# Kernel optimization log

Measured on AMD Instinct MI355X. Metric: run time of the kernel, lower is better.

The kernel has to match this reference:

```python
import jax, jax.numpy as jnp
import numpy as np

B, L, C, OUT = 8, 256, 512, 512


def setup_inputs() -> dict:
    key = jax.random.key(0)
    ks = jax.random.split(key, 8)
    xd = jax.random.normal(ks[0], (B, L, C), jnp.float32)
    xt = jax.random.normal(ks[1], (B, L, C), jnp.float32)
    # Linear weights stored (in, out): y = x @ W + b (equiv. to torch x @ W^T)
    Wc = jax.random.normal(ks[2], (C, C), jnp.float32) * 0.02
    bc = jnp.zeros((C,), jnp.float32)
    Wp = jax.random.normal(ks[3], (C, C), jnp.float32) * 0.02
    bp = jnp.zeros((C,), jnp.float32)
    Wf = jax.random.normal(ks[4], (C, OUT), jnp.float32) * 0.02
    bf = jnp.zeros((OUT,), jnp.float32)
    return {"xd": xd, "xt": xt, "Wc": Wc, "bc": bc, "Wp": Wp, "bp": bp, "Wf": Wf, "bf": bf}


def reference(xd, xt, Wc, bc, Wp, bp, Wf, bf):
    # projected features
    pt = jax.nn.relu(xt) @ Wp + bp              # (b, Lt, C)
    pc = jax.nn.relu(xd) @ Wc + bc              # (b, Ld, C)
    # sigmoid bilinear scores: (b, Lt, Ld) == (b, Ld, Lt) since Lt == Ld structurally
    scores = jax.nn.sigmoid(jnp.einsum('bic,bkc->bik', pt, pc))
    # normalize by total per-batch sum
    w = scores / jnp.sum(scores, axis=(1, 2), keepdims=True)
    # tanh of elementwise outer product, reduced with attention weights
    # cp[b,c] = sum_{i,j} tanh(xd[b,i,c] * xt[b,j,c]) * w[b,i,j]
    cp = jnp.einsum('bijc,bij->bc', jnp.tanh(xd[:, :, None, :] * xt[:, None, :, :]), w)
    return cp @ Wf + bf
```

## Files before the change

### kernel.cpp

```cpp
#include <hip/hip_runtime.h>
#include <math.h>

#define B_   8
#define L_   256
#define C_   512
#define OUT_ 512

typedef _Float16 half8 __attribute__((ext_vector_type(8)));
typedef _Float16 half4 __attribute__((ext_vector_type(4)));
typedef float    f32x4 __attribute__((ext_vector_type(4)));
typedef float    f32x2 __attribute__((ext_vector_type(2)));

__global__ __launch_bounds__(256)
void proj_mfma_kernel(const float* __restrict__ xt, const float* __restrict__ Wp,
                      const float* __restrict__ bp,
                      const float* __restrict__ xd, const float* __restrict__ Wc,
                      const float* __restrict__ bc,
                      _Float16* __restrict__ pt, _Float16* __restrict__ pc)
{
    const int which = blockIdx.z;
    const float* __restrict__ X    = which ? xd : xt;
    const float* __restrict__ W    = which ? Wc : Wp;
    const float* __restrict__ bias = which ? bc : bp;
    _Float16*    __restrict__ Y    = which ? pc : pt;

    __shared__ _Float16 Ah[2][64][40];
    __shared__ _Float16 Bh[2][64][40];
    __shared__ _Float16 Ot[64][72];

    const int tid = threadIdx.x;
    const int m0 = blockIdx.y << 6, n0 = blockIdx.x << 6;
    const int lane = tid & 63, wv = tid >> 6;
    const int l15 = lane & 15, quad = lane >> 4;

    const int srow = tid >> 2, sch = (tid & 3) << 3;
    const float* Ag = X + (size_t)(m0 + srow) * C_ + sch;
    const int nl = tid & 63, kseg = tid >> 6;
    const float* Bg = W + (size_t)(kseg << 3) * C_ + n0 + nl;

    float4 a0 = *(const float4*)(Ag);
    float4 a1 = *(const float4*)(Ag + 4);
    float wr[8];
    #pragma unroll
    for (int r = 0; r < 8; ++r) wr[r] = Bg[(size_t)r * C_];

    {
        half8 av;
        av[0] = (_Float16)fmaxf(a0.x, 0.f); av[1] = (_Float16)fmaxf(a0.y, 0.f);
        av[2] = (_Float16)fmaxf(a0.z, 0.f); av[3] = (_Float16)fmaxf(a0.w, 0.f);
        av[4] = (_Float16)fmaxf(a1.x, 0.f); av[5] = (_Float16)fmaxf(a1.y, 0.f);
        av[6] = (_Float16)fmaxf(a1.z, 0.f); av[7] = (_Float16)fmaxf(a1.w, 0.f);
        *(half8*)&Ah[0][srow][sch] = av;
        half8 bv;
        #pragma unroll
        for (int r = 0; r < 8; ++r) bv[r] = (_Float16)wr[r];
        *(half8*)&Bh[0][nl][kseg << 3] = bv;
    }

    f32x4 acc[4] = {};
    for (int ks = 0; ks < 16; ++ks) {
        const int cur = ks & 1;
        if (ks < 15) {
            Ag += 32;
            Bg += 32 * C_;
            a0 = *(const float4*)(Ag);
            a1 = *(const float4*)(Ag + 4);
            #pragma unroll
            for (int r = 0; r < 8; ++r) wr[r] = Bg[(size_t)r * C_];
        }
        __syncthreads();
        half8 af = *(const half8*)&Ah[cur][(wv << 4) + l15][quad << 3];
        #pragma unroll
        for (int nb = 0; nb < 4; ++nb) {
            half8 bf = *(const half8*)&Bh[cur][(nb << 4) + l15][quad << 3];
            acc[nb] = __builtin_amdgcn_mfma_f32_16x16x32_f16(af, bf, acc[nb], 0, 0, 0);
        }
        if (ks < 15) {
            half8 av;
            av[0] = (_Float16)fmaxf(a0.x, 0.f); av[1] = (_Float16)fmaxf(a0.y, 0.f);
            av[2] = (_Float16)fmaxf(a0.z, 0.f); av[3] = (_Float16)fmaxf(a0.w, 0.f);
            av[4] = (_Float16)fmaxf(a1.x, 0.f); av[5] = (_Float16)fmaxf(a1.y, 0.f);
            av[6] = (_Float16)fmaxf(a1.z, 0.f); av[7] = (_Float16)fmaxf(a1.w, 0.f);
            *(half8*)&Ah[cur ^ 1][srow][sch] = av;
            half8 bv;
            #pragma unroll
            for (int r = 0; r < 8; ++r) bv[r] = (_Float16)wr[r];
            *(half8*)&Bh[cur ^ 1][nl][kseg << 3] = bv;
        }
    }

    __syncthreads();
    #pragma unroll
    for (int nb = 0; nb < 4; ++nb) {
        const float bz = bias[n0 + (nb << 4) + l15];
        #pragma unroll
        for (int r = 0; r < 4; ++r)
            Ot[(wv << 4) + (quad << 2) + r][(nb << 4) + l15] = (_Float16)(acc[nb][r] + bz);
    }
    __syncthreads();
    const int erow = tid >> 3, ech = (tid & 7) << 3;
    #pragma unroll
    for (int h = 0; h < 64; h += 32)
        *(half8*)&Y[(size_t)(m0 + erow + h) * C_ + n0 + ech] = *(const half8*)&Ot[erow + h][ech];
}

__device__ __forceinline__ float sigmoid_fast(float z) {
    float e = __builtin_amdgcn_exp2f(-1.4426950408889634f * z);
    return __builtin_amdgcn_rcpf(e + 1.0f);
}

__global__ __launch_bounds__(512, 4)
void cp_scores_kernel(const _Float16* __restrict__ pt, const _Float16* __restrict__ pc,
                      const float* __restrict__ xd, const float* __restrict__ xt,
                      float* __restrict__ partials, float* __restrict__ sums_part)
{
    const int bx = blockIdx.x, by = blockIdx.y, b = blockIdx.z;
    const int i0 = bx << 5, j0 = by << 5;
    const int tid = threadIdx.x;
    const int lane = tid & 63, wv = tid >> 6;
    const int l15 = lane & 15, quad = lane >> 4;

    __shared__ _Float16 Ah[2][32][40];
    __shared__ _Float16 Bh[2][32][40];
    __shared__ float ws_[32][36];
    __shared__ float wred[4];

    const int sHalf = tid >> 8;
    const int srow  = (tid & 255) >> 3;
    const int sch   = (tid & 7) << 2;
    const _Float16* Sg = (sHalf ? pc + (size_t)(b * L_ + j0 + srow) * C_
                                : pt + (size_t)(b * L_ + i0 + srow) * C_) + sch;

    half4 v = *(const half4*)Sg;
    if (sHalf) *(half4*)&Bh[0][srow][sch] = v; else *(half4*)&Ah[0][srow][sch] = v;

    f32x4 acc = {};
    for (int ks = 0; ks < 16; ++ks) {
        const int cur = ks & 1;
        if (ks < 15) { Sg += 32; v = *(const half4*)Sg; }
        __syncthreads();
        if (wv < 4) {
            half8 af = *(const half8*)&Ah[cur][((wv >> 1) << 4) + l15][quad << 3];
            half8 bf = *(const half8*)&Bh[cur][((wv & 1) << 4) + l15][quad << 3];
            acc = __builtin_amdgcn_mfma_f32_16x16x32_f16(af, bf, acc, 0, 0, 0);
        }
        if (ks < 15) {
            if (sHalf) *(half4*)&Bh[cur ^ 1][srow][sch] = v;
            else       *(half4*)&Ah[cur ^ 1][srow][sch] = v;
        }
    }

    float lsum = 0.f;
    if (wv < 4) {
        const int n = ((wv & 1) << 4) + l15;
        const int m = ((wv >> 1) << 4) + (quad << 2);
        float4 sg;
        sg.x = sigmoid_fast(acc[0]);
        sg.y = sigmoid_fast(acc[1]);
        sg.z = sigmoid_fast(acc[2]);
        sg.w = sigmoid_fast(acc[3]);
        *(float4*)&ws_[n][m] = sg;
        lsum = (sg.x + sg.y) + (sg.z + sg.w);
    }
    #pragma unroll
    for (int off = 32; off; off >>= 1) lsum += __shfl_xor(lsum, off);
    if (wv < 4 && lane == 0) wred[wv] = lsum;
    __syncthreads();
    if (tid == 0)
        sums_part[(b << 6) | (bx << 3) | by] = (wred[0] + wred[1]) + (wred[2] + wred[3]);

    const int c = tid;
    const float* __restrict__ xdb = xd + (size_t)(b * L_ + i0) * C_ + c;
    const float* __restrict__ xtb = xt + (size_t)(b * L_ + j0) * C_ + c;
    f32x2 xds2[16];
    float xtv[32];
    #pragma unroll
    for (int i = 0; i < 16; ++i) {
        xds2[i].x = xdb[(size_t)(2 * i) * C_]     * 2.8853900817779268f;
        xds2[i].y = xdb[(size_t)(2 * i + 1) * C_] * 2.8853900817779268f;
    }
    #pragma unroll
    for (int j = 0; j < 32; ++j)
        xtv[j] = xtb[(size_t)j * C_];

    f32x2 acc01 = {0.f, 0.f}, acc23 = {0.f, 0.f};
    for (int jj = 0; jj < 32; ++jj) {
        const float xv = xtv[jj];
        #pragma unroll
        for (int i = 0; i < 32; i += 4) {
            const float4 w4 = *(const float4*)&ws_[jj][i];
            f32x2 x01 = xds2[i >> 1] * xv;
            f32x2 e01 = { __builtin_amdgcn_exp2f(x01.x), __builtin_amdgcn_exp2f(x01.y) };
            f32x2 q01 = e01 + 1.0f;
            float rp01 = __builtin_amdgcn_rcpf(q01.x * q01.y);
            f32x2 r01 = rp01 * __builtin_shufflevector(q01, q01, 1, 0);
            f32x2 w01 = { w4.x, w4.y };
            acc01 = w01 * r01 + acc01;
            f32x2 x23 = xds2[(i >> 1) + 1] * xv;
            f32x2 e23 = { __builtin_amdgcn_exp2f(x23.x), __builtin_amdgcn_exp2f(x23.y) };
            f32x2 q23 = e23 + 1.0f;
            float rp23 = __builtin_amdgcn_rcpf(q23.x * q23.y);
            f32x2 r23 = rp23 * __builtin_shufflevector(q23, q23, 1, 0);
            f32x2 w23 = { w4.z, w4.w };
            acc23 = w23 * r23 + acc23;
        }
    }
    const int p = (bx << 3) | by;
    partials[(size_t)((b << 6) | p) * C_ + c] =
        (acc01.x + acc01.y) + (acc23.x + acc23.y);
}

__global__ __launch_bounds__(512)
void finalize_kernel(const float* __restrict__ partials, const float* __restrict__ sums_part,
                     const float* __restrict__ Wf, const float* __restrict__ bfv,
                     float* __restrict__ out)
{
    const int b = blockIdx.y;
    const int t = threadIdx.x;
    __shared__ float cp[C_];
    __shared__ float red[512];
    __shared__ float sumsh;

    red[t] = (t < 64) ? sums_part[(b << 6) | t] : 0.f;

    float s = 0.f;
    #pragma unroll
    for (int p = 0; p < 64; ++p)
        s += partials[(size_t)((b << 6) | p) * C_ + t];

    __syncthreads();
    for (int st = 256; st > 0; st >>= 1) {
        if (t < st) red[t] += red[t + st];
        __syncthreads();
    }
    if (t == 0) sumsh = red[0];
    __syncthreads();

    cp[t] = 1.0f - 2.0f * s / sumsh;
    __syncthreads();

    const int o  = ((int)blockIdx.x << 6) | (t & 63);
    const int c0 = (t >> 6) << 6;
    float acc = 0.f;
    #pragma unroll 8
    for (int i = 0; i < 64; ++i) {
        const int cc = c0 + i;
        acc = fmaf(cp[cc], Wf[(size_t)cc * OUT_ + o], acc);
    }
    red[t] = acc;
    __syncthreads();
    if (t < 64) {
        float a = 0.f;
        #pragma unroll
        for (int g = 0; g < 8; ++g) a += red[(g << 6) | t];
        out[(size_t)b * OUT_ + o] = a + bfv[o];
    }
}

extern "C" void kernel_launch(void* const* d_in, const int* in_sizes, int n_in,
                              void* d_out, int out_size, void* d_ws, size_t ws_size,
                              hipStream_t stream)
{
    const float* xd = (const float*)d_in[0];
    const float* xt = (const float*)d_in[1];
    const float* Wc = (const float*)d_in[2];
    const float* bc = (const float*)d_in[3];
    const float* Wp = (const float*)d_in[4];
    const float* bp = (const float*)d_in[5];
    const float* Wf = (const float*)d_in[6];
    const float* bf = (const float*)d_in[7];
    float* out = (float*)d_out;

    _Float16* pt  = (_Float16*)d_ws;
    _Float16* pc  = pt + 1048576;
    float* partials  = (float*)(pc + 1048576);
    float* sums_part = partials + B_ * 64 * C_;

    proj_mfma_kernel<<<dim3(8, 32, 2), 256, 0, stream>>>(xt, Wp, bp, xd, Wc, bc, pt, pc);
    cp_scores_kernel<<<dim3(8, 8, 8), 512, 0, stream>>>(pt, pc, xd, xt, partials, sums_part);
    finalize_kernel<<<dim3(8, 8), 512, 0, stream>>>(partials, sums_part, Wf, bf, out);
}
```

Baseline: 138.1 us.

## Split scores and tanh reduction into separate kernels with smaller tiles

The fused scores+tanh kernel is split in two. A scores kernel computes the sigmoid bilinear scores with MFMA, loading operands directly from global memory instead of through double-buffered LDS, and writes them to a workspace. A tanh kernel then uses 16x16 tiles, giving four times as many blocks and fewer registers per thread, which is meant to raise occupancy on the transcendental-heavy loop. In exchange it adds an extra launch, a round trip of the score matrix through global memory, and four times as many partials for finalize to reduce.

```diff
diff --git a/kernel.cpp b/kernel.cpp
--- a/kernel.cpp
+++ b/kernel.cpp
@@ -109,85 +109,92 @@
     return __builtin_amdgcn_rcpf(e + 1.0f);
 }
 
-__global__ __launch_bounds__(512, 4)
-void cp_scores_kernel(const _Float16* __restrict__ pt, const _Float16* __restrict__ pc,
-                      const float* __restrict__ xd, const float* __restrict__ xt,
-                      float* __restrict__ partials, float* __restrict__ sums_part)
+__global__ __launch_bounds__(256)
+void scores_kernel(const _Float16* __restrict__ pt, const _Float16* __restrict__ pc,
+                   float* __restrict__ w, float* __restrict__ sums_part)
 {
     const int bx = blockIdx.x, by = blockIdx.y, b = blockIdx.z;
     const int i0 = bx << 5, j0 = by << 5;
     const int tid = threadIdx.x;
     const int lane = tid & 63, wv = tid >> 6;
     const int l15 = lane & 15, quad = lane >> 4;
-
-    __shared__ _Float16 Ah[2][32][40];
-    __shared__ _Float16 Bh[2][32][40];
-    __shared__ float ws_[32][36];
+    const int mq = wv >> 1, nq = wv & 1;
+
     __shared__ float wred[4];
 
-    const int sHalf = tid >> 8;
-    const int srow  = (tid & 255) >> 3;
-    const int sch   = (tid & 7) << 2;
-    const _Float16* Sg = (sHalf ? pc + (size_t)(b * L_ + j0 + srow) * C_
-                                : pt + (size_t)(b * L_ + i0 + srow) * C_) + sch;
-
-    half4 v = *(const half4*)Sg;
-    if (sHalf) *(half4*)&Bh[0][srow][sch] = v; else *(half4*)&Ah[0][srow][sch] = v;
+    const _Float16* __restrict__ Ap =
+        pt + (size_t)(b * L_ + i0 + mq * 16 + l15) * C_ + (quad << 3);
+    const _Float16* __restrict__ Bp =
+        pc + (size_t)(b * L_ + j0 + nq * 16 + l15) * C_ + (quad << 3);
 
     f32x4 acc = {};
+    #pragma unroll
     for (int ks = 0; ks < 16; ++ks) {
-        const int cur = ks & 1;
-        if (ks < 15) { Sg += 32; v = *(const half4*)Sg; }
-        __syncthreads();
-        if (wv < 4) {
-            half8 af = *(const half8*)&Ah[cur][((wv >> 1) << 4) + l15][quad << 3];
-            half8 bf = *(const half8*)&Bh[cur][((wv & 1) << 4) + l15][quad << 3];
-            acc = __builtin_amdgcn_mfma_f32_16x16x32_f16(af, bf, acc, 0, 0, 0);
-        }
-        if (ks < 15) {
-            if (sHalf) *(half4*)&Bh[cur ^ 1][srow][sch] = v;
-            else       *(half4*)&Ah[cur ^ 1][srow][sch] = v;
-        }
-    }
-
-    float lsum = 0.f;
-    if (wv < 4) {
-        const int n = ((wv & 1) << 4) + l15;
-        const int m = ((wv >> 1) << 4) + (quad << 2);
-        float4 sg;
-        sg.x = sigmoid_fast(acc[0]);
-        sg.y = sigmoid_fast(acc[1]);
-        sg.z = sigmoid_fast(acc[2]);
-        sg.w = sigmoid_fast(acc[3]);
-        *(float4*)&ws_[n][m] = sg;
-        lsum = (sg.x + sg.y) + (sg.z + sg.w);
-    }
+        half8 af = *(const half8*)(Ap + (ks << 5));
+        half8 bf = *(const half8*)(Bp + (ks << 5));
+        acc = __builtin_amdgcn_mfma_f32_16x16x32_f16(af, bf, acc, 0, 0, 0);
+    }
+
+    float4 sg;
+    sg.x = sigmoid_fast(acc[0]);
+    sg.y = sigmoid_fast(acc[1]);
+    sg.z = sigmoid_fast(acc[2]);
+    sg.w = sigmoid_fast(acc[3]);
+
+    float* __restrict__ wp =
+        w + (size_t)(b * L_ + i0 + mq * 16 + (quad << 2)) * L_ + j0 + nq * 16 + l15;
+    wp[0 * L_] = sg.x;
+    wp[1 * L_] = sg.y;
+    wp[2 * L_] = sg.z;
+    wp[3 * L_] = sg.w;
+
+    float lsum = (sg.x + sg.y) + (sg.z + sg.w);
     #pragma unroll
     for (int off = 32; off; off >>= 1) lsum += __shfl_xor(lsum, off);
-    if (wv < 4 && lane == 0) wred[wv] = lsum;
+    if (lane == 0) wred[wv] = lsum;
     __syncthreads();
     if (tid == 0)
         sums_part[(b << 6) | (bx << 3) | by] = (wred[0] + wred[1]) + (wred[2] + wred[3]);
+}
+
+__global__ __launch_bounds__(512, 8)
+void tanh_cp_kernel(const float* __restrict__ w, const float* __restrict__ xd,
+                    const float* __restrict__ xt, float* __restrict__ partials)
+{
+    const int bx = blockIdx.x, by = blockIdx.y, b = blockIdx.z;
+    const int i0 = bx << 4, j0 = by << 4;
+    const int tid = threadIdx.x;
+
+    __shared__ float ws_[16][20];
+
+    if (tid < 64) {
+        const int ir = tid >> 2, j4 = (tid & 3) << 2;
+        const float4 v = *(const float4*)(w + (size_t)(b * L_ + i0 + ir) * L_ + j0 + j4);
+        ws_[j4 + 0][ir] = v.x;
+        ws_[j4 + 1][ir] = v.y;
+        ws_[j4 + 2][ir] = v.z;
+        ws_[j4 + 3][ir] = v.w;
+    }
 
     const int c = tid;
     const float* __restrict__ xdb = xd + (size_t)(b * L_ + i0) * C_ + c;
     const float* __restrict__ xtb = xt + (size_t)(b * L_ + j0) * C_ + c;
-    f32x2 xds2[16];
-    float xtv[32];
-    #pragma unroll
-    for (int i = 0; i < 16; ++i) {
-        xds2[i].x = xdb[(size_t)(2 * i) * C_]     * 2.8853900817779268f;
-        xds2[i].y = xdb[(size_t)(2 * i + 1) * C_] * 2.8853900817779268f;
-    }
-    #pragma unroll
-    for (int j = 0; j < 32; ++j)
-        xtv[j] = xtb[(size_t)j * C_];
+
+    f32x2 xds2[8];
+    #pragma unroll
+    for (int i = 0; i < 8; ++i) {
+        xds2[i].x = xdb[(size_t)(2 * i) * C_];
+        xds2[i].y = xdb[(size_t)(2 * i + 1) * C_];
+    }
+
+    __syncthreads();
 
     f32x2 acc01 = {0.f, 0.f}, acc23 = {0.f, 0.f};
-    for (int jj = 0; jj < 32; ++jj) {
-        const float xv = xtv[jj];
-        #pragma unroll
-        for (int i = 0; i < 32; i += 4) {
+    #pragma unroll
+    for (int jj = 0; jj < 16; ++jj) {
+        const float xv = xtb[(size_t)jj * C_] * 2.8853900817779268f;
+        #pragma unroll
+        for (int i = 0; i < 16; i += 4) {
             const float4 w4 = *(const float4*)&ws_[jj][i];
             f32x2 x01 = xds2[i >> 1] * xv;
             f32x2 e01 = { __builtin_amdgcn_exp2f(x01.x), __builtin_amdgcn_exp2f(x01.y) };
@@ -205,8 +212,8 @@
             acc23 = w23 * r23 + acc23;
         }
     }
-    const int p = (bx << 3) | by;
-    partials[(size_t)((b << 6) | p) * C_ + c] =
+    const int p = (bx << 4) | by;
+    partials[(size_t)((b << 8) | p) * C_ + c] =
         (acc01.x + acc01.y) + (acc23.x + acc23.y);
 }
 
@@ -224,9 +231,9 @@
     red[t] = (t < 64) ? sums_part[(b << 6) | t] : 0.f;
 
     float s = 0.f;
-    #pragma unroll
-    for (int p = 0; p < 64; ++p)
-        s += partials[(size_t)((b << 6) | p) * C_ + t];
+    #pragma unroll 8
+    for (int p = 0; p < 256; ++p)
+        s += partials[(size_t)((b << 8) | p) * C_ + t];
 
     __syncthreads();
     for (int st = 256; st > 0; st >>= 1) {
@@ -271,12 +278,14 @@
     const float* bf = (const float*)d_in[7];
     float* out = (float*)d_out;
 
-    _Float16* pt  = (_Float16*)d_ws;
-    _Float16* pc  = pt + 1048576;
-    float* partials  = (float*)(pc + 1048576);
-    float* sums_part = partials + B_ * 64 * C_;
+    _Float16* pt = (_Float16*)d_ws;
+    _Float16* pc = pt + 1048576;
+    float* w         = (float*)(pc + 1048576);
+    float* partials  = w + 524288;
+    float* sums_part = partials + 1048576;
 
     proj_mfma_kernel<<<dim3(8, 32, 2), 256, 0, stream>>>(xt, Wp, bp, xd, Wc, bc, pt, pc);
-    cp_scores_kernel<<<dim3(8, 8, 8), 512, 0, stream>>>(pt, pc, xd, xt, partials, sums_part);
+    scores_kernel<<<dim3(8, 8, 8), 256, 0, stream>>>(pt, pc, w, sums_part);
+    tanh_cp_kernel<<<dim3(16, 16, 8), 512, 0, stream>>>(w, xd, xt, partials);
     finalize_kernel<<<dim3(8, 8), 512, 0, stream>>>(partials, sums_part, Wf, bf, out);
 }
```

Result: slower. 151.6 us (+9.7%).
